# Optimization experiments

Measured on AMD Instinct MI355X. Metric: run time of the kernel, lower is better.

The kernel has to match this reference:

```python
import jax, jax.numpy as jnp
import numpy as np

B, LP, LR = 16, 128, 1024
D = 128
DG = 640  # 5 * 128 concat
K = 7     # number of FC trans heads
EDGE_P = 0.05


def _gcn_block(x, adj, mask, W1, b1, W2, b2):
    # x: [B,L,DG], adj: [B,L,L] (nonzero => edge weight 1, like dense_to_sparse + GCNConv)
    A = (adj != 0).astype(x.dtype)
    L = A.shape[-1]
    eye = jnp.eye(L, dtype=x.dtype)
    Ah = jnp.maximum(A, eye)                     # add_remaining_self_loops
    deg = Ah.sum(axis=1)                         # col degree [B,L] (gcn_norm uses target index)
    dinv = jax.lax.rsqrt(deg)                    # deg >= 1 thanks to self loops
    N = Ah * dinv[:, :, None] * dinv[:, None, :] # normalized adjacency per edge (r,c)
    agg = lambda h: jnp.einsum('brc,brd->bcd', N, h)  # aggregate sources r into target c
    h1 = jax.nn.relu(agg(x @ W1) + b1)
    h2 = agg(h1 @ W2) + b2
    return jax.nn.relu(x + h2) * mask[..., None]


def _fc_trans(feature, Wt, bt):
    # feature: [B,L,DG]; Wt: [K,D,DG]; bt: [K,D]
    h = jnp.einsum('bld,kod->kblo', feature, Wt) + bt[:, None, None, :]
    h = jax.nn.relu(h)                 # FCNet [640->128], ReLU (dropout off in eval)
    return jnp.swapaxes(h, 2, 3)       # [K,B,D,L] (transpose(1,2))


def _forward(x_pep, x_ss_pep, x_2_pep, x_dense_pep, x_pretrain_pep,
             x_pro, x_ss_pro, x_2_pro, x_dense_pro, x_pretrain_pro,
             x_edge_pep, x_edge_pro, x_seqmask_pep, x_seqmask_pro,
             E_seq, E_ss, E_two, W_dpep, b_dpep, W_dpro, b_dpro,
             W_ppep, b_ppep, W_ppro, b_ppro,
             Wg_pep1, bg_pep1, Wg_pep2, bg_pep2,
             Wg_pro1, bg_pro1, Wg_pro2, bg_pro2,
             Wt_pep, bt_pep, Wt_pro, bt_pro):
    enc_pep = jnp.concatenate([
        E_seq[x_pep], E_ss[x_ss_pep], E_two[x_2_pep],
        x_dense_pep @ W_dpep + b_dpep,
        x_pretrain_pep @ W_ppep + b_ppep], axis=-1) * x_seqmask_pep[..., None]
    enc_pro = jnp.concatenate([
        E_seq[x_pro], E_ss[x_ss_pro], E_two[x_2_pro],
        x_dense_pro @ W_dpro + b_dpro,
        x_pretrain_pro @ W_ppro + b_ppro], axis=-1) * x_seqmask_pro[..., None]

    f_pep = _gcn_block(enc_pep, x_edge_pep, x_seqmask_pep, Wg_pep1, bg_pep1, Wg_pep2, bg_pep2)
    f_pro = _gcn_block(enc_pro, x_edge_pro, x_seqmask_pro, Wg_pro1, bg_pro1, Wg_pro2, bg_pro2)

    pep_vecs = _fc_trans(f_pep, Wt_pep, bt_pep)[..., None]        # [K,B,D,LP,1] (unsqueeze 3)
    pro_vecs = _fc_trans(f_pro, Wt_pro, bt_pro)[:, :, :, None, :]  # [K,B,D,1,LR] (unsqueeze 2)
    return pep_vecs, pro_vecs


def setup_inputs() -> dict:
    key = jax.random.key(0)
    ks = jax.random.split(key, 40)
    f32 = jnp.float32
    s = 0.05
    inp = {
        'x_pep': jax.random.randint(ks[0], (B, LP), 0, 25),
        'x_ss_pep': jax.random.randint(ks[1], (B, LP), 0, 73),
        'x_2_pep': jax.random.randint(ks[2], (B, LP), 0, 8),
        'x_dense_pep': jax.random.normal(ks[3], (B, LP, 3), f32),
        'x_pretrain_pep': jax.random.normal(ks[4], (B, LP, 1024), f32),
        'x_pro': jax.random.randint(ks[5], (B, LR), 0, 25),
        'x_ss_pro': jax.random.randint(ks[6], (B, LR), 0, 73),
        'x_2_pro': jax.random.randint(ks[7], (B, LR), 0, 8),
        'x_dense_pro': jax.random.normal(ks[8], (B, LR, 23), f32),
        'x_pretrain_pro': jax.random.normal(ks[9], (B, LR, 1024), f32),
        'x_edge_pep': (jax.random.uniform(ks[10], (B, LP, LP)) < EDGE_P).astype(f32),
        'x_edge_pro': (jax.random.uniform(ks[11], (B, LR, LR)) < EDGE_P).astype(f32),
        'x_seqmask_pep': jnp.ones((B, LP), f32),
        'x_seqmask_pro': jnp.ones((B, LR), f32),
        'E_seq': jax.random.normal(ks[12], (25, D), f32) * s,
        'E_ss': jax.random.normal(ks[13], (73, D), f32) * s,
        'E_two': jax.random.normal(ks[14], (8, D), f32) * s,
        'W_dpep': jax.random.normal(ks[15], (3, D), f32) * s,
        'b_dpep': jnp.zeros((D,), f32),
        'W_dpro': jax.random.normal(ks[16], (23, D), f32) * s,
        'b_dpro': jnp.zeros((D,), f32),
        'W_ppep': jax.random.normal(ks[17], (1024, D), f32) * s,
        'b_ppep': jnp.zeros((D,), f32),
        'W_ppro': jax.random.normal(ks[18], (1024, D), f32) * s,
        'b_ppro': jnp.zeros((D,), f32),
        'Wg_pep1': jax.random.normal(ks[19], (DG, DG), f32) * s,
        'bg_pep1': jnp.zeros((DG,), f32),
        'Wg_pep2': jax.random.normal(ks[20], (DG, DG), f32) * s,
        'bg_pep2': jnp.zeros((DG,), f32),
        'Wg_pro1': jax.random.normal(ks[21], (DG, DG), f32) * s,
        'bg_pro1': jnp.zeros((DG,), f32),
        'Wg_pro2': jax.random.normal(ks[22], (DG, DG), f32) * s,
        'bg_pro2': jnp.zeros((DG,), f32),
        'Wt_pep': jax.random.normal(ks[23], (K, D, DG), f32) * s,
        'bt_pep': jnp.zeros((K, D), f32),
        'Wt_pro': jax.random.normal(ks[24], (K, D, DG), f32) * s,
        'bt_pro': jnp.zeros((K, D), f32),
    }
    return inp


def reference(x_pep, x_ss_pep, x_2_pep, x_dense_pep, x_pretrain_pep,
              x_pro, x_ss_pro, x_2_pro, x_dense_pro, x_pretrain_pro,
              x_edge_pep, x_edge_pro, x_seqmask_pep, x_seqmask_pro,
              E_seq, E_ss, E_two, W_dpep, b_dpep, W_dpro, b_dpro,
              W_ppep, b_ppep, W_ppro, b_ppro,
              Wg_pep1, bg_pep1, Wg_pep2, bg_pep2,
              Wg_pro1, bg_pro1, Wg_pro2, bg_pro2,
              Wt_pep, bt_pep, Wt_pro, bt_pro):
    return _forward(x_pep, x_ss_pep, x_2_pep, x_dense_pep, x_pretrain_pep,
                    x_pro, x_ss_pro, x_2_pro, x_dense_pro, x_pretrain_pro,
                    x_edge_pep, x_edge_pro, x_seqmask_pep, x_seqmask_pro,
                    E_seq, E_ss, E_two, W_dpep, b_dpep, W_dpro, b_dpro,
                    W_ppep, b_ppep, W_ppro, b_ppro,
                    Wg_pep1, bg_pep1, Wg_pep2, bg_pep2,
                    Wg_pro1, bg_pro1, Wg_pro2, bg_pro2,
                    Wt_pep, bt_pep, Wt_pro, bt_pro)
```

## Files before the change

kernel.cpp:

```cpp
#include <hip/hip_runtime.h>
#include <hip/hip_bf16.h>

#define BSZ 16
#define LP 128
#define LR 1024
#define DD 128
#define DG 640
#define KH 7
#define SPLITK 4

typedef __bf16 bf16x8 __attribute__((ext_vector_type(8)));
typedef __bf16 bf16x4v __attribute__((ext_vector_type(4)));
typedef float f32x4 __attribute__((ext_vector_type(4)));
typedef unsigned int uint32;

__device__ __forceinline__ void mfma_core_n64(
    const ushort* __restrict__ Ab, int lda,
    const ushort* __restrict__ Bb, int ldb,
    int m0, int n0, int kStart, int kEnd, f32x4 (&acc)[2][4]) {
  __shared__ __align__(16) ushort As[128 * 72];
  __shared__ __align__(16) ushort Bs[64 * 72];
  int t = threadIdx.x;
  int wave = t >> 6, lane = t & 63;
  int quad = lane >> 4, l16 = lane & 15;
  int wm = wave * 32;
  int r1 = t >> 2, o1 = (t & 3) * 16;

  int4 a0, a1, a2, a3, bb0, bb1;
  auto load_k = [&](int k0) {
    a0 = *(const int4*)(Ab + (size_t)(m0 + r1) * lda + k0 + o1);
    a1 = *(const int4*)(Ab + (size_t)(m0 + r1) * lda + k0 + o1 + 8);
    a2 = *(const int4*)(Ab + (size_t)(m0 + r1 + 64) * lda + k0 + o1);
    a3 = *(const int4*)(Ab + (size_t)(m0 + r1 + 64) * lda + k0 + o1 + 8);
    bb0 = *(const int4*)(Bb + (size_t)(n0 + r1) * ldb + k0 + o1);
    bb1 = *(const int4*)(Bb + (size_t)(n0 + r1) * ldb + k0 + o1 + 8);
  };

  load_k(kStart);
  for (int k0 = kStart; k0 < kEnd; k0 += 64) {
    __syncthreads();
    *(int4*)&As[r1 * 72 + o1] = a0;
    *(int4*)&As[r1 * 72 + o1 + 8] = a1;
    *(int4*)&As[(r1 + 64) * 72 + o1] = a2;
    *(int4*)&As[(r1 + 64) * 72 + o1 + 8] = a3;
    *(int4*)&Bs[r1 * 72 + o1] = bb0;
    *(int4*)&Bs[r1 * 72 + o1 + 8] = bb1;
    __syncthreads();
    if (k0 + 64 < kEnd) load_k(k0 + 64);
    #pragma unroll
    for (int kc = 0; kc < 2; ++kc) {
      bf16x8 af[2], bfr[4];
      #pragma unroll
      for (int fi = 0; fi < 2; ++fi)
        af[fi] = *(const bf16x8*)&As[(wm + fi * 16 + l16) * 72 + kc * 32 + quad * 8];
      #pragma unroll
      for (int fj = 0; fj < 4; ++fj)
        bfr[fj] = *(const bf16x8*)&Bs[(fj * 16 + l16) * 72 + kc * 32 + quad * 8];
      #pragma unroll
      for (int fi = 0; fi < 2; ++fi)
        #pragma unroll
        for (int fj = 0; fj < 4; ++fj)
          acc[fi][fj] = __builtin_amdgcn_mfma_f32_16x16x32_bf16(
              af[fi], bfr[fj], acc[fi][fj], 0, 0, 0);
    }
  }
}

__device__ __forceinline__ void agg_core_n64(
    const uint32* __restrict__ pb, int L,
    const ushort* __restrict__ Bb, int ldb,
    int m0, int n0, f32x4 (&acc)[2][4]) {
  __shared__ __align__(16) ushort Bs[64 * 72];
  __shared__ uint32 Aw[2][128];
  int t = threadIdx.x;
  int wave = t >> 6, lane = t & 63;
  int quad = lane >> 4, l16 = lane & 15;
  int wm = wave * 32;
  int r1 = t >> 2, o1 = (t & 3) * 16;
  int half = t >> 7, cc = t & 127;

  int4 bb0, bb1;
  uint32 w;
  auto load_k = [&](int k0) {
    bb0 = *(const int4*)(Bb + (size_t)(n0 + r1) * ldb + k0 + o1);
    bb1 = *(const int4*)(Bb + (size_t)(n0 + r1) * ldb + k0 + o1 + 8);
    w = pb[(size_t)((k0 >> 5) + half) * L + m0 + cc];
  };

  load_k(0);
  for (int k0 = 0; k0 < L; k0 += 64) {
    __syncthreads();
    *(int4*)&Bs[r1 * 72 + o1] = bb0;
    *(int4*)&Bs[r1 * 72 + o1 + 8] = bb1;
    Aw[half][cc] = w;
    __syncthreads();
    if (k0 + 64 < L) load_k(k0 + 64);
    #pragma unroll
    for (int kc = 0; kc < 2; ++kc) {
      bf16x8 af[2], bfr[4];
      #pragma unroll
      for (int fj = 0; fj < 4; ++fj)
        bfr[fj] = *(const bf16x8*)&Bs[(fj * 16 + l16) * 72 + kc * 32 + quad * 8];
      #pragma unroll
      for (int fi = 0; fi < 2; ++fi) {
        uint32 bits = (Aw[kc][wm + fi * 16 + l16] >> (quad * 8)) & 0xffu;
        int4 p;
        p.x = (int)((((bits >> 0) & 1) ? 0x3F80u : 0u) | (((bits >> 1) & 1) ? 0x3F800000u : 0u));
        p.y = (int)((((bits >> 2) & 1) ? 0x3F80u : 0u) | (((bits >> 3) & 1) ? 0x3F800000u : 0u));
        p.z = (int)((((bits >> 4) & 1) ? 0x3F80u : 0u) | (((bits >> 5) & 1) ? 0x3F800000u : 0u));
        p.w = (int)((((bits >> 6) & 1) ? 0x3F80u : 0u) | (((bits >> 7) & 1) ? 0x3F800000u : 0u));
        af[fi] = *(bf16x8*)&p;
      }
      #pragma unroll
      for (int fi = 0; fi < 2; ++fi)
        #pragma unroll
        for (int fj = 0; fj < 4; ++fj)
          acc[fi][fj] = __builtin_amdgcn_mfma_f32_16x16x32_bf16(
              af[fi], bfr[fj], acc[fi][fj], 0, 0, 0);
    }
  }
}

__device__ __forceinline__ void mfma_core_f32_m64(
    const float* __restrict__ Af, int lda,
    const ushort* __restrict__ Bb, int ldb,
    int m0, int kStart, int kEnd, f32x4 (&acc)[2][4]) {
  __shared__ __align__(16) ushort As[64 * 72];
  __shared__ __align__(16) ushort Bs[128 * 72];
  int t = threadIdx.x;
  int wave = t >> 6, lane = t & 63;
  int quad = lane >> 4, l16 = lane & 15;
  int wm = (wave >> 1) * 32, wn = (wave & 1) * 64;
  int r1 = t >> 2, o1 = (t & 3) * 16;

  int4 b00, b01, b10, b11;
  float4 af32[4];

  auto load_k = [&](int k0) {
    b00 = *(const int4*)(Bb + (size_t)r1 * ldb + k0 + o1);
    b01 = *(const int4*)(Bb + (size_t)r1 * ldb + k0 + o1 + 8);
    b10 = *(const int4*)(Bb + (size_t)(r1 + 64) * ldb + k0 + o1);
    b11 = *(const int4*)(Bb + (size_t)(r1 + 64) * ldb + k0 + o1 + 8);
    #pragma unroll
    for (int s = 0; s < 4; ++s) {
      int idx = t + s * 256;
      int row = idx >> 4, c4 = (idx & 15) * 4;
      af32[s] = *(const float4*)(Af + (size_t)(m0 + row) * lda + k0 + c4);
    }
  };

  load_k(kStart);
  for (int k0 = kStart; k0 < kEnd; k0 += 64) {
    __syncthreads();
    #pragma unroll
    for (int s = 0; s < 4; ++s) {
      int idx = t + s * 256;
      int row = idx >> 4, c4 = (idx & 15) * 4;
      ushort4 u; __bf16 h;
      h = (__bf16)af32[s].x; u.x = *(ushort*)&h;
      h = (__bf16)af32[s].y; u.y = *(ushort*)&h;
      h = (__bf16)af32[s].z; u.z = *(ushort*)&h;
      h = (__bf16)af32[s].w; u.w = *(ushort*)&h;
      *(ushort4*)&As[row * 72 + c4] = u;
    }
    *(int4*)&Bs[r1 * 72 + o1] = b00;
    *(int4*)&Bs[r1 * 72 + o1 + 8] = b01;
    *(int4*)&Bs[(r1 + 64) * 72 + o1] = b10;
    *(int4*)&Bs[(r1 + 64) * 72 + o1 + 8] = b11;
    __syncthreads();
    if (k0 + 64 < kEnd) load_k(k0 + 64);
    #pragma unroll
    for (int kc = 0; kc < 2; ++kc) {
      bf16x8 af[2], bfr[4];
      #pragma unroll
      for (int fi = 0; fi < 2; ++fi)
        af[fi] = *(const bf16x8*)&As[(wm + fi * 16 + l16) * 72 + kc * 32 + quad * 8];
      #pragma unroll
      for (int fj = 0; fj < 4; ++fj)
        bfr[fj] = *(const bf16x8*)&Bs[(wn + fj * 16 + l16) * 72 + kc * 32 + quad * 8];
      #pragma unroll
      for (int fi = 0; fi < 2; ++fi)
        #pragma unroll
        for (int fj = 0; fj < 4; ++fj)
          acc[fi][fj] = __builtin_amdgcn_mfma_f32_16x16x32_bf16(
              af[fi], bfr[fj], acc[fi][fj], 0, 0, 0);
    }
  }
}

__device__ __forceinline__ void tr_tile(const float* __restrict__ src,
                                        __bf16* __restrict__ dst,
                                        int R, int C, int cb, int rb, int t) {
  __shared__ float T[32][33];
  int r0 = rb * 32, c0 = cb * 32;
  #pragma unroll
  for (int s = 0; s < 4; ++s) {
    int idx = t + s * 256;
    int r = idx >> 5, c = idx & 31;
    T[r][c] = src[(size_t)(r0 + r) * C + c0 + c];
  }
  __syncthreads();
  #pragma unroll
  for (int s = 0; s < 4; ++s) {
    int idx = t + s * 256;
    int c = idx >> 5, r = idx & 31;
    dst[(size_t)(c0 + c) * R + r0 + r] = (__bf16)T[r][c];
  }
}

__global__ __launch_bounds__(256) void prep_weights(
    const float* __restrict__ Wppep, const float* __restrict__ Wppro,
    const float* __restrict__ Wg1p, const float* __restrict__ Wg2p,
    const float* __restrict__ Wg1r, const float* __restrict__ Wg2r,
    const float* __restrict__ Wtp, const float* __restrict__ Wtr,
    __bf16* __restrict__ WppTp, __bf16* __restrict__ WppTr,
    __bf16* __restrict__ Wg1Tp, __bf16* __restrict__ Wg2Tp,
    __bf16* __restrict__ Wg1Tr, __bf16* __restrict__ Wg2Tr,
    __bf16* __restrict__ WtBp, __bf16* __restrict__ WtBr) {
  int z = blockIdx.z, bx = blockIdx.x, t = threadIdx.x;
  if (z < 2) {
    if (bx >= 128) return;
    tr_tile(z ? Wppro : Wppep, z ? WppTr : WppTp, 1024, 128, bx % 4, bx / 4, t);
  } else if (z < 6) {
    if (bx >= 400) return;
    const float* src = (z == 2) ? Wg1p : (z == 3) ? Wg2p : (z == 4) ? Wg1r : Wg2r;
    __bf16* dst = (z == 2) ? Wg1Tp : (z == 3) ? Wg2Tp : (z == 4) ? Wg1Tr : Wg2Tr;
    tr_tile(src, dst, 640, 640, bx % 20, bx / 20, t);
  } else {
    if (bx >= 560) return;
    const float* src = (z == 6) ? Wtp : Wtr;
    __bf16* dst = (z == 6) ? WtBp : WtBr;
    int i = bx * 256 + t;
    float4 v = ((const float4*)src)[i];
    bf16x4v o;
    o.x = (__bf16)v.x; o.y = (__bf16)v.y; o.z = (__bf16)v.z; o.w = (__bf16)v.w;
    ((bf16x4v*)dst)[i] = o;
  }
}

__global__ __launch_bounds__(256) void prep_pack_merged(
    const float* __restrict__ adjP, const float* __restrict__ adjR,
    uint32* __restrict__ packedP, uint32* __restrict__ packedR,
    float* __restrict__ degP, float* __restrict__ degR) {
  int t = threadIdx.x;
  const float* adj; uint32* packed; float* deg;
  int b, rw, c, L;
  if (blockIdx.z < 16) {
    L = LR; b = blockIdx.z; rw = blockIdx.y; c = blockIdx.x * 256 + t;
    adj = adjR; packed = packedR; deg = degR;
  } else {
    L = LP; b = blockIdx.y; rw = blockIdx.x; c = t;
    if (b >= 16 || c >= LP) return;
    adj = adjP; packed = packedP; deg = degP;
  }
  const float* adjB = adj + (size_t)b * L * L;
  uint32 w = 0;
  int rbase = rw * 32;
  #pragma unroll 8
  for (int j = 0; j < 32; ++j) {
    float a = adjB[(size_t)(rbase + j) * L + c];
    if (a != 0.f || (rbase + j) == c) w |= (1u << j);
  }
  packed[((size_t)b * (L >> 5) + rw) * L + c] = w;
  atomicAdd(deg + b * L + c, (float)__popc(w));
}

__global__ __launch_bounds__(256) void pre_gemm(
    const float* __restrict__ XpP, const float* __restrict__ XpR,
    const __bf16* __restrict__ WppTp, const __bf16* __restrict__ WppTr,
    float* __restrict__ partP, float* __restrict__ partR) {
  int bx = blockIdx.x, s = blockIdx.y;
  int pep = bx < (BSZ * LP / 64);
  int m0 = (pep ? bx : bx - BSZ * LP / 64) * 64;
  const float* A = pep ? XpP : XpR;
  const ushort* B = (const ushort*)(pep ? WppTp : WppTr);
  int BL = pep ? BSZ * LP : BSZ * LR;
  float* part = (pep ? partP : partR) + (size_t)s * BL * DD;

  f32x4 acc[2][4];
  #pragma unroll
  for (int i = 0; i < 2; ++i)
    #pragma unroll
    for (int j = 0; j < 4; ++j) acc[i][j] = (f32x4){0.f, 0.f, 0.f, 0.f};
  mfma_core_f32_m64(A, 1024, B, 1024, m0, s * (1024 / SPLITK),
                    (s + 1) * (1024 / SPLITK), acc);

  int t = threadIdx.x;
  int wave = t >> 6, lane = t & 63;
  int quad = lane >> 4, l16 = lane & 15;
  int wm = (wave >> 1) * 32, wn = (wave & 1) * 64;
  #pragma unroll
  for (int fi = 0; fi < 2; ++fi)
    #pragma unroll
    for (int r = 0; r < 4; ++r) {
      int m = m0 + wm + fi * 16 + quad * 4 + r;
      #pragma unroll
      for (int fj = 0; fj < 4; ++fj) {
        int n = wn + fj * 16 + l16;
        part[(size_t)m * DD + n] = acc[fi][fj][r];
      }
    }
}

__global__ __launch_bounds__(128) void encoder_merged(
    const int* __restrict__ xsP, const int* __restrict__ xssP,
    const int* __restrict__ x2P, const float* __restrict__ xdP,
    const float* __restrict__ WdP, const float* __restrict__ bdP,
    const float* __restrict__ maskP, const float* __restrict__ partP,
    const float* __restrict__ bppP, __bf16* __restrict__ encP,
    const int* __restrict__ xsR, const int* __restrict__ xssR,
    const int* __restrict__ x2R, const float* __restrict__ xdR,
    const float* __restrict__ WdR, const float* __restrict__ bdR,
    const float* __restrict__ maskR, const float* __restrict__ partR,
    const float* __restrict__ bppR, __bf16* __restrict__ encR,
    const float* __restrict__ Eseq, const float* __restrict__ Ess,
    const float* __restrict__ Etwo) {
  int gw = blockIdx.x;
  int t = threadIdx.x;
  int pep = gw < BSZ * LP;
  int row = pep ? gw : gw - BSZ * LP;
  int BL = pep ? BSZ * LP : BSZ * LR;
  int Kd = pep ? 3 : 23;
  const int* xs = pep ? xsP : xsR;
  const int* xss = pep ? xssP : xssR;
  const int* x2 = pep ? x2P : x2R;
  const float* xd = pep ? xdP : xdR;
  const float* Wd = pep ? WdP : WdR;
  const float* bd = pep ? bdP : bdR;
  const float* mask = pep ? maskP : maskR;
  const float* part = pep ? partP : partR;
  const float* bpp = pep ? bppP : bppR;
  __bf16* enc = pep ? encP : encR;

  float m = mask[row];
  int i0 = xs[row], i1 = xss[row], i2 = x2[row];
  __bf16* e = enc + (size_t)row * DG;
  e[t]        = (__bf16)(Eseq[i0 * DD + t] * m);
  e[DD + t]   = (__bf16)(Ess[i1 * DD + t] * m);
  e[2*DD + t] = (__bf16)(Etwo[i2 * DD + t] * m);
  float acc = bd[t];
  const float* xr = xd + (size_t)row * Kd;
  for (int i = 0; i < Kd; ++i) acc = fmaf(xr[i], Wd[i * DD + t], acc);
  e[3*DD + t] = (__bf16)(acc * m);
  float p = bpp[t];
  #pragma unroll
  for (int s = 0; s < SPLITK; ++s)
    p += part[(size_t)s * BL * DD + (size_t)row * DD + t];
  e[4*DD + t] = (__bf16)(p * m);
}

__global__ __launch_bounds__(256) void linT_merged(
    const __bf16* __restrict__ WgTp, const __bf16* __restrict__ srcP,
    const float* __restrict__ degP, __bf16* __restrict__ dstP,
    const __bf16* __restrict__ WgTr, const __bf16* __restrict__ srcR,
    const float* __restrict__ degR, __bf16* __restrict__ dstR) {
  int bx = blockIdx.x;
  int pep = bx < (BSZ * LP / 64);
  int n0 = (pep ? bx : bx - BSZ * LP / 64) * 64;
  int m0 = blockIdx.y * 128;
  int BL = pep ? BSZ * LP : BSZ * LR;
  const ushort* A = (const ushort*)(pep ? WgTp : WgTr);
  const ushort* B = (const ushort*)(pep ? srcP : srcR);
  const float* deg = pep ? degP : degR;
  __bf16* dst = pep ? dstP : dstR;

  f32x4 acc[2][4];
  #pragma unroll
  for (int i = 0; i < 2; ++i)
    #pragma unroll
    for (int j = 0; j < 4; ++j) acc[i][j] = (f32x4){0.f, 0.f, 0.f, 0.f};
  mfma_core_n64(A, DG, B, DG, m0, n0, 0, DG, acc);

  int t = threadIdx.x;
  int wave = t >> 6, lane = t & 63;
  int quad = lane >> 4, l16 = lane & 15;
  int wm = wave * 32;
  #pragma unroll
  for (int fi = 0; fi < 2; ++fi)
    #pragma unroll
    for (int r = 0; r < 4; ++r) {
      int m = m0 + wm + fi * 16 + quad * 4 + r;
      #pragma unroll
      for (int fj = 0; fj < 4; ++fj) {
        int n = n0 + fj * 16 + l16;
        dst[(size_t)m * BL + n] = (__bf16)(acc[fi][fj][r] * rsqrtf(deg[n]));
      }
    }
}

__global__ __launch_bounds__(256) void agg_merged(
    const uint32* __restrict__ packedP, const __bf16* __restrict__ XtP,
    const float* __restrict__ degP, const float* __restrict__ biasP,
    const __bf16* __restrict__ encEP, const float* __restrict__ maskP,
    __bf16* __restrict__ YP,
    const uint32* __restrict__ packedR, const __bf16* __restrict__ XtR,
    const float* __restrict__ degR, const float* __restrict__ biasR,
    const __bf16* __restrict__ encER, const float* __restrict__ maskR,
    __bf16* __restrict__ YR) {
  int bx = blockIdx.x;
  int b = bx / 10;
  int n0 = (bx % 10) * 64;
  int pep = (blockIdx.y == 0);
  int L = pep ? LP : LR;
  int BL = BSZ * L;
  int m0 = pep ? 0 : (blockIdx.y - 1) * 128;
  const uint32* pb = (pep ? packedP : packedR) + (size_t)b * (L >> 5) * L;
  const ushort* Bb = (const ushort*)(pep ? XtP : XtR) + (size_t)b * L;
  const float* deg = pep ? degP : degR;
  const float* bias = pep ? biasP : biasR;
  const __bf16* encE = pep ? encEP : encER;
  const float* mask = pep ? maskP : maskR;
  __bf16* Y = pep ? YP : YR;

  f32x4 acc[2][4];
  #pragma unroll
  for (int i = 0; i < 2; ++i)
    #pragma unroll
    for (int j = 0; j < 4; ++j) acc[i][j] = (f32x4){0.f, 0.f, 0.f, 0.f};
  agg_core_n64(pb, L, Bb, BL, m0, n0, acc);

  int t = threadIdx.x;
  int wave = t >> 6, lane = t & 63;
  int quad = lane >> 4, l16 = lane & 15;
  int wm = wave * 32;
  int gRow = b * L;
  #pragma unroll
  for (int fi = 0; fi < 2; ++fi)
    #pragma unroll
    for (int r = 0; r < 4; ++r) {
      int m = m0 + wm + fi * 16 + quad * 4 + r;
      int gi = gRow + m;
      float di = rsqrtf(deg[gi]);
      float rm = mask ? mask[gi] : 1.f;
      #pragma unroll
      for (int fj = 0; fj < 4; ++fj) {
        int n = n0 + fj * 16 + l16;
        float v = acc[fi][fj][r] * di + bias[n];
        if (encE) v += (float)encE[(size_t)gi * DG + n];
        v = fmaxf(v, 0.f);
        v *= rm;
        Y[(size_t)gi * DG + n] = (__bf16)v;
      }
    }
}

__global__ __launch_bounds__(256) void fct_merged(
    const __bf16* __restrict__ WtBp, const float* __restrict__ btp,
    const __bf16* __restrict__ Yp, float* __restrict__ outP,
    const __bf16* __restrict__ WtBr, const float* __restrict__ btr,
    const __bf16* __restrict__ Yr, float* __restrict__ outR) {
  int kh = blockIdx.y;
  int pro = (blockIdx.z < 16);
  const ushort* A;
  const ushort* B;
  const float* bt;
  int n0;
  if (pro) {
    A = (const ushort*)(WtBr + (size_t)kh * DD * DG);
    B = (const ushort*)(Yr + (size_t)blockIdx.z * LR * DG);
    bt = btr;
    n0 = blockIdx.x * 64;
  } else {
    A = (const ushort*)(WtBp + (size_t)kh * DD * DG);
    B = (const ushort*)Yp;
    bt = btp;
    n0 = ((blockIdx.z - 16) * 16 + blockIdx.x) * 64;
  }

  f32x4 acc[2][4];
  #pragma unroll
  for (int i = 0; i < 2; ++i)
    #pragma unroll
    for (int j = 0; j < 4; ++j) acc[i][j] = (f32x4){0.f, 0.f, 0.f, 0.f};
  mfma_core_n64(A, DG, B, DG, 0, n0, 0, DG, acc);

  int t = threadIdx.x;
  int wave = t >> 6, lane = t & 63;
  int quad = lane >> 4, l16 = lane & 15;
  int wm = wave * 32;
  #pragma unroll
  for (int fi = 0; fi < 2; ++fi)
    #pragma unroll
    for (int r = 0; r < 4; ++r) {
      int m = wm + fi * 16 + quad * 4 + r;
      float bb = bt[kh * DD + m];
      #pragma unroll
      for (int fj = 0; fj < 4; ++fj) {
        int n = n0 + fj * 16 + l16;
        float v = fmaxf(acc[fi][fj][r] + bb, 0.f);
        if (pro) {
          outR[((size_t)(kh * BSZ + blockIdx.z) * DD + m) * LR + n] = v;
        } else {
          int b = n >> 7, l = n & 127;
          outP[((size_t)(kh * BSZ + b) * DD + m) * LP + l] = v;
        }
      }
    }
}

extern "C" void kernel_launch(void* const* d_in, const int* in_sizes, int n_in,
                              void* d_out, int out_size, void* d_ws, size_t ws_size,
                              hipStream_t stream) {
  const int*   x_pep          = (const int*)d_in[0];
  const int*   x_ss_pep       = (const int*)d_in[1];
  const int*   x_2_pep        = (const int*)d_in[2];
  const float* x_dense_pep    = (const float*)d_in[3];
  const float* x_pretrain_pep = (const float*)d_in[4];
  const int*   x_pro          = (const int*)d_in[5];
  const int*   x_ss_pro       = (const int*)d_in[6];
  const int*   x_2_pro        = (const int*)d_in[7];
  const float* x_dense_pro    = (const float*)d_in[8];
  const float* x_pretrain_pro = (const float*)d_in[9];
  const float* x_edge_pep     = (const float*)d_in[10];
  const float* x_edge_pro     = (const float*)d_in[11];
  const float* mask_pep       = (const float*)d_in[12];
  const float* mask_pro       = (const float*)d_in[13];
  const float* E_seq          = (const float*)d_in[14];
  const float* E_ss           = (const float*)d_in[15];
  const float* E_two          = (const float*)d_in[16];
  const float* W_dpep         = (const float*)d_in[17];
  const float* b_dpep         = (const float*)d_in[18];
  const float* W_dpro         = (const float*)d_in[19];
  const float* b_dpro         = (const float*)d_in[20];
  const float* W_ppep         = (const float*)d_in[21];
  const float* b_ppep         = (const float*)d_in[22];
  const float* W_ppro         = (const float*)d_in[23];
  const float* b_ppro         = (const float*)d_in[24];
  const float* Wg_pep1        = (const float*)d_in[25];
  const float* bg_pep1        = (const float*)d_in[26];
  const float* Wg_pep2        = (const float*)d_in[27];
  const float* bg_pep2        = (const float*)d_in[28];
  const float* Wg_pro1        = (const float*)d_in[29];
  const float* bg_pro1        = (const float*)d_in[30];
  const float* Wg_pro2        = (const float*)d_in[31];
  const float* bg_pro2        = (const float*)d_in[32];
  const float* Wt_pep         = (const float*)d_in[33];
  const float* bt_pep         = (const float*)d_in[34];
  const float* Wt_pro         = (const float*)d_in[35];
  const float* bt_pro         = (const float*)d_in[36];

  float* out = (float*)d_out;
  const int BLp = BSZ * LP;
  const int BLr = BSZ * LR;
  const size_t out_pro_off = (size_t)KH * BSZ * DD * LP;

  char* w = (char*)d_ws;
  __bf16* encBp  = (__bf16*)w; w += (size_t)BLp * DG * 2;
  __bf16* encBr  = (__bf16*)w; w += (size_t)BLr * DG * 2;
  __bf16* bufATp = (__bf16*)w; w += (size_t)DG * BLp * 2;
  __bf16* bufATr = (__bf16*)w; w += (size_t)DG * BLr * 2;
  __bf16* bufYp  = (__bf16*)w; w += (size_t)BLp * DG * 2;
  __bf16* bufYr  = (__bf16*)w; w += (size_t)BLr * DG * 2;
  __bf16* WppTp  = (__bf16*)w; w += (size_t)DD * 1024 * 2;
  __bf16* WppTr  = (__bf16*)w; w += (size_t)DD * 1024 * 2;
  __bf16* Wg1Tp  = (__bf16*)w; w += (size_t)DG * DG * 2;
  __bf16* Wg2Tp  = (__bf16*)w; w += (size_t)DG * DG * 2;
  __bf16* Wg1Tr  = (__bf16*)w; w += (size_t)DG * DG * 2;
  __bf16* Wg2Tr  = (__bf16*)w; w += (size_t)DG * DG * 2;
  __bf16* WtBp   = (__bf16*)w; w += (size_t)KH * DD * DG * 2;
  __bf16* WtBr   = (__bf16*)w; w += (size_t)KH * DD * DG * 2;
  uint32* packedP = (uint32*)w; w += (size_t)BSZ * (LP / 32) * LP * 4;
  uint32* packedR = (uint32*)w; w += (size_t)BSZ * (LR / 32) * LR * 4;
  float* degP  = (float*)w; w += (size_t)BLp * 4;
  float* degR  = (float*)w; w += (size_t)BLr * 4;
  float* partP = (float*)w; w += (size_t)SPLITK * BLp * DD * 4;
  float* partR = (float*)w; w += (size_t)SPLITK * BLr * DD * 4;

  prep_weights<<<dim3(560, 1, 8), 256, 0, stream>>>(
      W_ppep, W_ppro, Wg_pep1, Wg_pep2, Wg_pro1, Wg_pro2, Wt_pep, Wt_pro,
      WppTp, WppTr, Wg1Tp, Wg2Tp, Wg1Tr, Wg2Tr, WtBp, WtBr);
  hipMemsetAsync(degP, 0, (size_t)(BLp + BLr) * sizeof(float), stream);
  prep_pack_merged<<<dim3(4, 32, 17), 256, 0, stream>>>(
      x_edge_pep, x_edge_pro, packedP, packedR, degP, degR);
  pre_gemm<<<dim3((BLp + BLr) / 64, SPLITK), 256, 0, stream>>>(
      x_pretrain_pep, x_pretrain_pro, WppTp, WppTr, partP, partR);
  encoder_merged<<<BLp + BLr, 128, 0, stream>>>(
      x_pep, x_ss_pep, x_2_pep, x_dense_pep, W_dpep, b_dpep, mask_pep, partP,
      b_ppep, encBp,
      x_pro, x_ss_pro, x_2_pro, x_dense_pro, W_dpro, b_dpro, mask_pro, partR,
      b_ppro, encBr,
      E_seq, E_ss, E_two);
  linT_merged<<<dim3((BLp + BLr) / 64, DG / 128), 256, 0, stream>>>(
      Wg1Tp, encBp, degP, bufATp, Wg1Tr, encBr, degR, bufATr);
  agg_merged<<<dim3(160, 9), 256, 0, stream>>>(
      packedP, bufATp, degP, bg_pep1, nullptr, nullptr, bufYp,
      packedR, bufATr, degR, bg_pro1, nullptr, nullptr, bufYr);
  linT_merged<<<dim3((BLp + BLr) / 64, DG / 128), 256, 0, stream>>>(
      Wg2Tp, bufYp, degP, bufATp, Wg2Tr, bufYr, degR, bufATr);
  agg_merged<<<dim3(160, 9), 256, 0, stream>>>(
      packedP, bufATp, degP, bg_pep2, encBp, mask_pep, bufYp,
      packedR, bufATr, degR, bg_pro2, encBr, mask_pro, bufYr);
  fct_merged<<<dim3(16, KH, 18), 256, 0, stream>>>(
      WtBp, bt_pep, bufYp, out,
      WtBr, bt_pro, bufYr, out + out_pro_off);
}
```

Measured before the change: 447.2 us.

## Merge weight prep and adjacency packing into one kernel, compute dinv in encoder

Weight transpose/convert and adjacency bit-packing now share a single flat-grid launch, which removes one kernel launch and the memset. Column degrees are no longer built with atomics during packing. The encoder recounts them from the packed words with popc plus a warp shuffle and stores rsqrt(deg) once. Downstream GEMM and aggregation kernels read the precomputed inverse sqrt instead of calling rsqrtf on every element. The encoder gains a strided read of the packed words per row.

```diff
diff --git a/kernel.cpp b/kernel.cpp
--- a/kernel.cpp
+++ b/kernel.cpp
@@ -208,52 +208,9 @@
   }
 }
 
-__global__ __launch_bounds__(256) void prep_weights(
-    const float* __restrict__ Wppep, const float* __restrict__ Wppro,
-    const float* __restrict__ Wg1p, const float* __restrict__ Wg2p,
-    const float* __restrict__ Wg1r, const float* __restrict__ Wg2r,
-    const float* __restrict__ Wtp, const float* __restrict__ Wtr,
-    __bf16* __restrict__ WppTp, __bf16* __restrict__ WppTr,
-    __bf16* __restrict__ Wg1Tp, __bf16* __restrict__ Wg2Tp,
-    __bf16* __restrict__ Wg1Tr, __bf16* __restrict__ Wg2Tr,
-    __bf16* __restrict__ WtBp, __bf16* __restrict__ WtBr) {
-  int z = blockIdx.z, bx = blockIdx.x, t = threadIdx.x;
-  if (z < 2) {
-    if (bx >= 128) return;
-    tr_tile(z ? Wppro : Wppep, z ? WppTr : WppTp, 1024, 128, bx % 4, bx / 4, t);
-  } else if (z < 6) {
-    if (bx >= 400) return;
-    const float* src = (z == 2) ? Wg1p : (z == 3) ? Wg2p : (z == 4) ? Wg1r : Wg2r;
-    __bf16* dst = (z == 2) ? Wg1Tp : (z == 3) ? Wg2Tp : (z == 4) ? Wg1Tr : Wg2Tr;
-    tr_tile(src, dst, 640, 640, bx % 20, bx / 20, t);
-  } else {
-    if (bx >= 560) return;
-    const float* src = (z == 6) ? Wtp : Wtr;
-    __bf16* dst = (z == 6) ? WtBp : WtBr;
-    int i = bx * 256 + t;
-    float4 v = ((const float4*)src)[i];
-    bf16x4v o;
-    o.x = (__bf16)v.x; o.y = (__bf16)v.y; o.z = (__bf16)v.z; o.w = (__bf16)v.w;
-    ((bf16x4v*)dst)[i] = o;
-  }
-}
-
-__global__ __launch_bounds__(256) void prep_pack_merged(
-    const float* __restrict__ adjP, const float* __restrict__ adjR,
-    uint32* __restrict__ packedP, uint32* __restrict__ packedR,
-    float* __restrict__ degP, float* __restrict__ degR) {
-  int t = threadIdx.x;
-  const float* adj; uint32* packed; float* deg;
-  int b, rw, c, L;
-  if (blockIdx.z < 16) {
-    L = LR; b = blockIdx.z; rw = blockIdx.y; c = blockIdx.x * 256 + t;
-    adj = adjR; packed = packedR; deg = degR;
-  } else {
-    L = LP; b = blockIdx.y; rw = blockIdx.x; c = t;
-    if (b >= 16 || c >= LP) return;
-    adj = adjP; packed = packedP; deg = degP;
-  }
-  const float* adjB = adj + (size_t)b * L * L;
+__device__ __forceinline__ void pack_col(const float* __restrict__ adjB,
+                                         uint32* __restrict__ packed,
+                                         int L, int b, int rw, int c) {
   uint32 w = 0;
   int rbase = rw * 32;
   #pragma unroll 8
@@ -262,7 +219,49 @@
     if (a != 0.f || (rbase + j) == c) w |= (1u << j);
   }
   packed[((size_t)b * (L >> 5) + rw) * L + c] = w;
-  atomicAdd(deg + b * L + c, (float)__popc(w));
+}
+
+__global__ __launch_bounds__(256) void prep_all(
+    const float* __restrict__ Wppep, const float* __restrict__ Wppro,
+    const float* __restrict__ Wg1p, const float* __restrict__ Wg2p,
+    const float* __restrict__ Wg1r, const float* __restrict__ Wg2r,
+    const float* __restrict__ Wtp, const float* __restrict__ Wtr,
+    const float* __restrict__ adjP, const float* __restrict__ adjR,
+    __bf16* __restrict__ WppTp, __bf16* __restrict__ WppTr,
+    __bf16* __restrict__ Wg1Tp, __bf16* __restrict__ Wg2Tp,
+    __bf16* __restrict__ Wg1Tr, __bf16* __restrict__ Wg2Tr,
+    __bf16* __restrict__ WtBp, __bf16* __restrict__ WtBr,
+    uint32* __restrict__ packedP, uint32* __restrict__ packedR) {
+  int g = blockIdx.x, t = threadIdx.x;
+  if (g < 256) {
+    int zi = g >> 7, bx = g & 127;
+    tr_tile(zi ? Wppro : Wppep, zi ? WppTr : WppTp, 1024, 128, bx % 4, bx / 4, t);
+  } else if (g < 1856) {
+    int u = g - 256;
+    int zi = u / 400, bx = u % 400;
+    const float* src = (zi == 0) ? Wg1p : (zi == 1) ? Wg2p : (zi == 2) ? Wg1r : Wg2r;
+    __bf16* dst = (zi == 0) ? Wg1Tp : (zi == 1) ? Wg2Tp : (zi == 2) ? Wg1Tr : Wg2Tr;
+    tr_tile(src, dst, 640, 640, bx % 20, bx / 20, t);
+  } else if (g < 2976) {
+    int u = g - 1856;
+    int zi = u / 560, bx = u % 560;
+    const float* src = zi ? Wtr : Wtp;
+    __bf16* dst = zi ? WtBr : WtBp;
+    int i = bx * 256 + t;
+    float4 v = ((const float4*)src)[i];
+    bf16x4v o;
+    o.x = (__bf16)v.x; o.y = (__bf16)v.y; o.z = (__bf16)v.z; o.w = (__bf16)v.w;
+    ((bf16x4v*)dst)[i] = o;
+  } else if (g < 5024) {
+    int u = g - 2976;
+    int b = u >> 7, rem = u & 127;
+    int rw = rem >> 2, c = (rem & 3) * 256 + t;
+    pack_col(adjR + (size_t)b * LR * LR, packedR, LR, b, rw, c);
+  } else {
+    int u = g - 5024;
+    if (t >= LP) return;
+    pack_col(adjP + (size_t)(u >> 2) * LP * LP, packedP, LP, u >> 2, u & 3, t);
+  }
 }
 
 __global__ __launch_bounds__(256) void pre_gemm(
@@ -308,17 +307,20 @@
     const float* __restrict__ WdP, const float* __restrict__ bdP,
     const float* __restrict__ maskP, const float* __restrict__ partP,
     const float* __restrict__ bppP, __bf16* __restrict__ encP,
+    const uint32* __restrict__ packedP, float* __restrict__ dinvP,
     const int* __restrict__ xsR, const int* __restrict__ xssR,
     const int* __restrict__ x2R, const float* __restrict__ xdR,
     const float* __restrict__ WdR, const float* __restrict__ bdR,
     const float* __restrict__ maskR, const float* __restrict__ partR,
     const float* __restrict__ bppR, __bf16* __restrict__ encR,
+    const uint32* __restrict__ packedR, float* __restrict__ dinvR,
     const float* __restrict__ Eseq, const float* __restrict__ Ess,
     const float* __restrict__ Etwo) {
   int gw = blockIdx.x;
   int t = threadIdx.x;
   int pep = gw < BSZ * LP;
   int row = pep ? gw : gw - BSZ * LP;
+  int L = pep ? LP : LR;
   int BL = pep ? BSZ * LP : BSZ * LR;
   int Kd = pep ? 3 : 23;
   const int* xs = pep ? xsP : xsR;
@@ -330,7 +332,19 @@
   const float* mask = pep ? maskP : maskR;
   const float* part = pep ? partP : partR;
   const float* bpp = pep ? bppP : bppR;
+  const uint32* packed = pep ? packedP : packedR;
+  float* dinv = pep ? dinvP : dinvR;
   __bf16* enc = pep ? encP : encR;
+
+  int nw = L >> 5;
+  int bb = row / L, ccol = row % L;
+  uint32 wv = (t < nw) ? packed[((size_t)bb * nw + t) * L + ccol] : 0u;
+  int cnt = __popc(wv);
+  if (t < 64) {
+    #pragma unroll
+    for (int off = 16; off >= 1; off >>= 1) cnt += __shfl_down(cnt, off);
+    if (t == 0) dinv[row] = rsqrtf((float)cnt);
+  }
 
   float m = mask[row];
   int i0 = xs[row], i1 = xss[row], i2 = x2[row];
@@ -351,9 +365,9 @@
 
 __global__ __launch_bounds__(256) void linT_merged(
     const __bf16* __restrict__ WgTp, const __bf16* __restrict__ srcP,
-    const float* __restrict__ degP, __bf16* __restrict__ dstP,
+    const float* __restrict__ dinvP, __bf16* __restrict__ dstP,
     const __bf16* __restrict__ WgTr, const __bf16* __restrict__ srcR,
-    const float* __restrict__ degR, __bf16* __restrict__ dstR) {
+    const float* __restrict__ dinvR, __bf16* __restrict__ dstR) {
   int bx = blockIdx.x;
   int pep = bx < (BSZ * LP / 64);
   int n0 = (pep ? bx : bx - BSZ * LP / 64) * 64;
@@ -361,7 +375,7 @@
   int BL = pep ? BSZ * LP : BSZ * LR;
   const ushort* A = (const ushort*)(pep ? WgTp : WgTr);
   const ushort* B = (const ushort*)(pep ? srcP : srcR);
-  const float* deg = pep ? degP : degR;
+  const float* dinv = pep ? dinvP : dinvR;
   __bf16* dst = pep ? dstP : dstR;
 
   f32x4 acc[2][4];
@@ -383,18 +397,18 @@
       #pragma unroll
       for (int fj = 0; fj < 4; ++fj) {
         int n = n0 + fj * 16 + l16;
-        dst[(size_t)m * BL + n] = (__bf16)(acc[fi][fj][r] * rsqrtf(deg[n]));
+        dst[(size_t)m * BL + n] = (__bf16)(acc[fi][fj][r] * dinv[n]);
       }
     }
 }
 
 __global__ __launch_bounds__(256) void agg_merged(
     const uint32* __restrict__ packedP, const __bf16* __restrict__ XtP,
-    const float* __restrict__ degP, const float* __restrict__ biasP,
+    const float* __restrict__ dinvP, const float* __restrict__ biasP,
     const __bf16* __restrict__ encEP, const float* __restrict__ maskP,
     __bf16* __restrict__ YP,
     const uint32* __restrict__ packedR, const __bf16* __restrict__ XtR,
-    const float* __restrict__ degR, const float* __restrict__ biasR,
+    const float* __restrict__ dinvR, const float* __restrict__ biasR,
     const __bf16* __restrict__ encER, const float* __restrict__ maskR,
     __bf16* __restrict__ YR) {
   int bx = blockIdx.x;
@@ -406,7 +420,7 @@
   int m0 = pep ? 0 : (blockIdx.y - 1) * 128;
   const uint32* pb = (pep ? packedP : packedR) + (size_t)b * (L >> 5) * L;
   const ushort* Bb = (const ushort*)(pep ? XtP : XtR) + (size_t)b * L;
-  const float* deg = pep ? degP : degR;
+  const float* dinv = pep ? dinvP : dinvR;
   const float* bias = pep ? biasP : biasR;
   const __bf16* encE = pep ? encEP : encER;
   const float* mask = pep ? maskP : maskR;
@@ -430,7 +444,7 @@
     for (int r = 0; r < 4; ++r) {
       int m = m0 + wm + fi * 16 + quad * 4 + r;
       int gi = gRow + m;
-      float di = rsqrtf(deg[gi]);
+      float di = dinv[gi];
       float rm = mask ? mask[gi] : 1.f;
       #pragma unroll
       for (int fj = 0; fj < 4; ++fj) {
@@ -561,35 +575,34 @@
   __bf16* WtBr   = (__bf16*)w; w += (size_t)KH * DD * DG * 2;
   uint32* packedP = (uint32*)w; w += (size_t)BSZ * (LP / 32) * LP * 4;
   uint32* packedR = (uint32*)w; w += (size_t)BSZ * (LR / 32) * LR * 4;
-  float* degP  = (float*)w; w += (size_t)BLp * 4;
-  float* degR  = (float*)w; w += (size_t)BLr * 4;
+  float* dinvP = (float*)w; w += (size_t)BLp * 4;
+  float* dinvR = (float*)w; w += (size_t)BLr * 4;
   float* partP = (float*)w; w += (size_t)SPLITK * BLp * DD * 4;
   float* partR = (float*)w; w += (size_t)SPLITK * BLr * DD * 4;
 
-  prep_weights<<<dim3(560, 1, 8), 256, 0, stream>>>(
+  prep_all<<<5088, 256, 0, stream>>>(
       W_ppep, W_ppro, Wg_pep1, Wg_pep2, Wg_pro1, Wg_pro2, Wt_pep, Wt_pro,
-      WppTp, WppTr, Wg1Tp, Wg2Tp, Wg1Tr, Wg2Tr, WtBp, WtBr);
-  hipMemsetAsync(degP, 0, (size_t)(BLp + BLr) * sizeof(float), stream);
-  prep_pack_merged<<<dim3(4, 32, 17), 256, 0, stream>>>(
-      x_edge_pep, x_edge_pro, packedP, packedR, degP, degR);
+      x_edge_pep, x_edge_pro,
+      WppTp, WppTr, Wg1Tp, Wg2Tp, Wg1Tr, Wg2Tr, WtBp, WtBr,
+      packedP, packedR);
   pre_gemm<<<dim3((BLp + BLr) / 64, SPLITK), 256, 0, stream>>>(
       x_pretrain_pep, x_pretrain_pro, WppTp, WppTr, partP, partR);
   encoder_merged<<<BLp + BLr, 128, 0, stream>>>(
       x_pep, x_ss_pep, x_2_pep, x_dense_pep, W_dpep, b_dpep, mask_pep, partP,
-      b_ppep, encBp,
+      b_ppep, encBp, packedP, dinvP,
       x_pro, x_ss_pro, x_2_pro, x_dense_pro, W_dpro, b_dpro, mask_pro, partR,
-      b_ppro, encBr,
+      b_ppro, encBr, packedR, dinvR,
       E_seq, E_ss, E_two);
   linT_merged<<<dim3((BLp + BLr) / 64, DG / 128), 256, 0, stream>>>(
-      Wg1Tp, encBp, degP, bufATp, Wg1Tr, encBr, degR, bufATr);
+      Wg1Tp, encBp, dinvP, bufATp, Wg1Tr, encBr, dinvR, bufATr);
   agg_merged<<<dim3(160, 9), 256, 0, stream>>>(
-      packedP, bufATp, degP, bg_pep1, nullptr, nullptr, bufYp,
-      packedR, bufATr, degR, bg_pro1, nullptr, nullptr, bufYr);
+      packedP, bufATp, dinvP, bg_pep1, nullptr, nullptr, bufYp,
+      packedR, bufATr, dinvR, bg_pro1, nullptr, nullptr, bufYr);
   linT_merged<<<dim3((BLp + BLr) / 64, DG / 128), 256, 0, stream>>>(
-      Wg2Tp, bufYp, degP, bufATp, Wg2Tr, bufYr, degR, bufATr);
+      Wg2Tp, bufYp, dinvP, bufATp, Wg2Tr, bufYr, dinvR, bufATr);
   agg_merged<<<dim3(160, 9), 256, 0, stream>>>(
-      packedP, bufATp, degP, bg_pep2, encBp, mask_pep, bufYp,
-      packedR, bufATr, degR, bg_pro2, encBr, mask_pro, bufYr);
+      packedP, bufATp, dinvP, bg_pep2, encBp, mask_pep, bufYp,
+      packedR, bufATr, dinvR, bg_pro2, encBr, mask_pro, bufYr);
   fct_merged<<<dim3(16, KH, 18), 256, 0, stream>>>(
       WtBp, bt_pep, bufYp, out,
       WtBr, bt_pro, bufYr, out + out_pro_off);
```

New measurement: 446.5 us. About the same (-0.2%).
